# Kernel optimization log

Measured on AMD Instinct MI355X. Metric: run time of the kernel, lower is better.

The kernel has to match this reference:

```python
import jax, jax.numpy as jnp
import numpy as np

T, N, D, B, L = 4, 1_000_000, 4, 16_384, 50
TOTAL = B * L

def setup_inputs() -> dict:
    key = jax.random.key(0)
    k0, k1, k2, k3, k4 = jax.random.split(key, 5)
    tables = jax.random.normal(k0, (T, N, D), dtype=jnp.float32) * 0.01
    indices = jax.random.randint(k1, (T, TOTAL), 0, N)
    # sorted segment ids encode jagged bag boundaries (variable lengths per sample)
    segment_ids = jnp.sort(jax.random.randint(k2, (T, TOTAL), 0, B), axis=-1)
    W = jax.random.normal(k3, (1, D), dtype=jnp.float32) * (1.0 / np.sqrt(D))
    b = jax.random.normal(k4, (1,), dtype=jnp.float32) * 0.01
    return {"tables": tables, "W": W, "b": b, "indices": indices, "segment_ids": segment_ids}

def reference(tables, W, b, indices, segment_ids):
    # EmbeddingBagCollection: per-table gather + sum pooling over jagged bags
    def pool_one(tbl, idx, seg):
        rows = tbl[idx]                                   # [TOTAL, D] irregular gather
        return jax.ops.segment_sum(rows, seg, num_segments=B)  # [B, D]
    pooled = jax.vmap(pool_one)(tables, indices, segment_ids)  # [T, B, D]
    # to_dict() + per-key append + cat(dim=0)  ==  reshape stacking tables along batch
    sparse_features = pooled.reshape(T * B, D)            # [T*B, D]
    # over_arch Linear(4, 1)
    return sparse_features @ W.T + b                      # [T*B, 1]
```

## Files before the change

### kernel.cpp

```cpp
#include <hip/hip_runtime.h>

constexpr int T     = 4;
constexpr int NROWS = 1000000;
constexpr int B     = 16384;
constexpr int TOTAL = 16384 * 50;

typedef float    fv4 __attribute__((ext_vector_type(4)));
typedef int      iv2 __attribute__((ext_vector_type(2)));
typedef _Float16 h2  __attribute__((ext_vector_type(2)));


__global__ __launch_bounds__(256)
void produce_kernel(const fv4*   __restrict__ tables,
                    const float* __restrict__ Wp,
                    const float* __restrict__ bias,
                    h2*          __restrict__ p2,
                    float*       __restrict__ out) {
    const int i = blockIdx.x * 256 + threadIdx.x;
    if (i < T * NROWS / 2) {
        const float wx = Wp[0], wy = Wp[1], wz = Wp[2], ww = Wp[3];
        const fv4 a = tables[2 * i];
        const fv4 b = tables[2 * i + 1];
        const float pa = a.x * wx + a.y * wy + a.z * wz + a.w * ww;
        const float pb = b.x * wx + b.y * wy + b.z * wz + b.w * ww;
        h2 h; h.x = (_Float16)pa; h.y = (_Float16)pb;
        p2[i] = h;
    }
    if (i < T * B) out[i] = bias[0];
}

template<int CTRL, int ROW_MASK, int BANK_MASK>
__device__ __forceinline__ float dpp_add(float x) {
    const int t = __builtin_amdgcn_update_dpp(0, __float_as_int(x),
                                              CTRL, ROW_MASK, BANK_MASK, true);
    return x + __int_as_float(t);
}
__device__ __forceinline__ float wave64_incl_scan(float x) {
    x = dpp_add<0x111, 0xf, 0xf>(x);
    x = dpp_add<0x112, 0xf, 0xf>(x);
    x = dpp_add<0x114, 0xf, 0xf>(x);
    x = dpp_add<0x118, 0xf, 0xf>(x);
    x = dpp_add<0x142, 0xa, 0xf>(x);
    x = dpp_add<0x143, 0xc, 0xf>(x);
    return x;
}

__global__ __launch_bounds__(256)
void pool_kernel(const _Float16* __restrict__ p,
                 const iv2*      __restrict__ indices,
                 const iv2*      __restrict__ segids,
                 float*          __restrict__ out)
{
    const int xcd    = blockIdx.x & 7;
    const int t      = xcd >> 1;
    const int within = ((blockIdx.x >> 3) << 1) + (xcd & 1);
    const int q      = within * 256 + threadIdx.x;
    const int gq     = t * (TOTAL / 2) + q;
    const int lane   = threadIdx.x & 63;

    const iv2 s2 = segids[gq];
    const iv2 i2 = indices[gq];

    const _Float16* pt = p + t * NROWS;
    const float v0 = (float)pt[i2.x];
    const float v1 = (float)pt[i2.y];
    const int   s0 = s2.x, s1 = s2.y;

    const float a0 = v0;
    const float x  = v1 + (s1 == s0 ? v0 : 0.f);
    const int   key = s1;

    const float P = wave64_incl_scan(x);
    const float E = P - x;

    const int kprev = __shfl_up(key, 1, 64);
    const int snext = __shfl_down(s0, 1, 64);
    const bool head = (lane == 0) || (kprev != key);
    const unsigned long long mask = __ballot(head);

    const unsigned long long le = mask & (~0ULL >> (63 - lane));
    const int   F  = 63 - __builtin_clzll(le);
    const float Ef = __shfl(E, F, 64);

    const unsigned long long lt = lane ? (mask & (~0ULL >> (64 - lane))) : 1ULL;
    const int   Fp  = 63 - __builtin_clzll(lt);
    const float Efp = __shfl(E, Fp, 64);

    float* outt = out + t * B;

    if (s0 != s1) {
        const float carry = (lane > 0 && kprev == s0) ? (E - Efp) : 0.f;
        atomicAdd(&outt[s0], a0 + carry);
    }

    if (lane == 63 || snext != key) {
        atomicAdd(&outt[key], P - Ef);
    }
}

extern "C" void kernel_launch(void* const* d_in, const int* in_sizes, int n_in,
                              void* d_out, int out_size, void* d_ws, size_t ws_size,
                              hipStream_t stream) {
    const fv4*   tables  = (const fv4*)d_in[0];
    const float* W       = (const float*)d_in[1];
    const float* bias    = (const float*)d_in[2];
    const iv2*   indices = (const iv2*)d_in[3];
    const iv2*   segids  = (const iv2*)d_in[4];
    float*       out     = (float*)d_out;

    h2*       p2 = (h2*)d_ws;
    _Float16* p  = (_Float16*)d_ws;

    {
        int n = T * NROWS / 2;
        produce_kernel<<<(n + 255) / 256, 256, 0, stream>>>(tables, W, bias, p2, out);
    }
    {
        pool_kernel<<<6400, 256, 0, stream>>>(p, indices, segids, out);
    }
}
```

Before: 130.2 us.

## Process eight elements per thread in pool kernel with serial segmented prefix

Each thread now loads two 16-byte vectors of indices and segment ids (eight elements) and does a serial in-thread segmented reduction before the wave-level scan. Grid size drops by a factor of four. This cuts the number of scan, shuffle and ballot passes and the thread count, while raising per-thread gather parallelism and register use. It also adds a loop of possible atomics per thread, and fewer blocks may reduce occupancy and latency hiding for the random gathers.

```diff
diff --git a/kernel.cpp b/kernel.cpp
--- a/kernel.cpp
+++ b/kernel.cpp
@@ -6,7 +6,7 @@
 constexpr int TOTAL = 16384 * 50;
 
 typedef float    fv4 __attribute__((ext_vector_type(4)));
-typedef int      iv2 __attribute__((ext_vector_type(2)));
+typedef int      iv4 __attribute__((ext_vector_type(4)));
 typedef _Float16 h2  __attribute__((ext_vector_type(2)));
 
 
@@ -47,34 +47,55 @@
 
 __global__ __launch_bounds__(256)
 void pool_kernel(const _Float16* __restrict__ p,
-                 const iv2*      __restrict__ indices,
-                 const iv2*      __restrict__ segids,
+                 const iv4*      __restrict__ indices,
+                 const iv4*      __restrict__ segids,
                  float*          __restrict__ out)
 {
     const int xcd    = blockIdx.x & 7;
     const int t      = xcd >> 1;
     const int within = ((blockIdx.x >> 3) << 1) + (xcd & 1);
-    const int q      = within * 256 + threadIdx.x;
-    const int gq     = t * (TOTAL / 2) + q;
+    const int q4     = within * 512 + threadIdx.x * 2;
+    const int gq     = t * (TOTAL / 4) + q4;
     const int lane   = threadIdx.x & 63;
 
-    const iv2 s2 = segids[gq];
-    const iv2 i2 = indices[gq];
+    const iv4 sA = segids[gq];
+    const iv4 sB = segids[gq + 1];
+    const iv4 iA = indices[gq];
+    const iv4 iB = indices[gq + 1];
 
     const _Float16* pt = p + t * NROWS;
-    const float v0 = (float)pt[i2.x];
-    const float v1 = (float)pt[i2.y];
-    const int   s0 = s2.x, s1 = s2.y;
+    float v[8];
+    v[0] = (float)pt[iA.x]; v[1] = (float)pt[iA.y];
+    v[2] = (float)pt[iA.z]; v[3] = (float)pt[iA.w];
+    v[4] = (float)pt[iB.x]; v[5] = (float)pt[iB.y];
+    v[6] = (float)pt[iB.z]; v[7] = (float)pt[iB.w];
+    int s[8];
+    s[0] = sA.x; s[1] = sA.y; s[2] = sA.z; s[3] = sA.w;
+    s[4] = sB.x; s[5] = sB.y; s[6] = sB.z; s[7] = sB.w;
 
-    const float a0 = v0;
-    const float x  = v1 + (s1 == s0 ? v0 : 0.f);
-    const int   key = s1;
+    float qa[8];
+    {
+        float acc = 0.f;
+        #pragma unroll
+        for (int k = 0; k < 8; ++k) { acc += v[k]; qa[k] = acc; }
+    }
+
+    float x = v[7];
+    {
+        bool cont = true;
+        #pragma unroll
+        for (int k = 6; k >= 0; --k) {
+            cont = cont && (s[k] == s[7]);
+            if (cont) x += v[k];
+        }
+    }
+    const int key = s[7];
 
     const float P = wave64_incl_scan(x);
     const float E = P - x;
 
     const int kprev = __shfl_up(key, 1, 64);
-    const int snext = __shfl_down(s0, 1, 64);
+    const int snext = __shfl_down(s[0], 1, 64);
     const bool head = (lane == 0) || (kprev != key);
     const unsigned long long mask = __ballot(head);
 
@@ -88,9 +109,20 @@
 
     float* outt = out + t * B;
 
-    if (s0 != s1) {
-        const float carry = (lane > 0 && kprev == s0) ? (E - Efp) : 0.f;
-        atomicAdd(&outt[s0], a0 + carry);
+    const float carry = (lane > 0 && kprev == s[0]) ? (E - Efp) : 0.f;
+
+    {
+        float rstart = 0.f;
+        bool  first  = true;
+        #pragma unroll
+        for (int k = 0; k < 7; ++k) {
+            if (s[k] != s[k + 1]) {
+                const float sum = qa[k] - rstart + (first ? carry : 0.f);
+                atomicAdd(&outt[s[k]], sum);
+                rstart = qa[k];
+                first  = false;
+            }
+        }
     }
 
     if (lane == 63 || snext != key) {
@@ -104,8 +136,8 @@
     const fv4*   tables  = (const fv4*)d_in[0];
     const float* W       = (const float*)d_in[1];
     const float* bias    = (const float*)d_in[2];
-    const iv2*   indices = (const iv2*)d_in[3];
-    const iv2*   segids  = (const iv2*)d_in[4];
+    const iv4*   indices = (const iv4*)d_in[3];
+    const iv4*   segids  = (const iv4*)d_in[4];
     float*       out     = (float*)d_out;
 
     h2*       p2 = (h2*)d_ws;
@@ -116,6 +148,6 @@
         produce_kernel<<<(n + 255) / 256, 256, 0, stream>>>(tables, W, bias, p2, out);
     }
     {
-        pool_kernel<<<6400, 256, 0, stream>>>(p, indices, segids, out);
+        pool_kernel<<<1600, 256, 0, stream>>>(p, indices, segids, out);
     }
 }
```

After: 131.2 us. No clear change (+0.8%).
